# Kernel tuning notes

Measured on AMD Instinct MI355X. Metric: run time of the kernel, lower is better.

Reference implementation:

```python
import jax, jax.numpy as jnp
import numpy as np

ALPHA = 0.2          # LeakyReLU negative slope
NEG_BIG = -9e15      # mask value from original code


def setup_inputs() -> dict:
    key = jax.random.key(0)
    k1, k2, k3, k4 = jax.random.split(key, 4)
    B, N, F_in, F_out = 16, 1024, 256, 256
    x = jax.random.normal(k1, (B, N, F_in), dtype=jnp.float32)
    adj = jax.random.randint(k2, (B, N, N), 0, 2, dtype=jnp.int32)
    # xavier-uniform-like scales
    W = jax.random.normal(k3, (F_in, F_out), dtype=jnp.float32) * np.sqrt(2.0 / (F_in + F_out))
    a = jax.random.normal(k4, (2 * F_out, 1), dtype=jnp.float32) * np.sqrt(2.0 / (2 * F_out + 1))
    return {"x": x, "adj": adj, "W": W, "a": a}


def reference(x, adj, W, a):
    # x: [B,N,Fin], adj: [B,N,N] (int mask), W: [Fin,Fout], a: [2*Fout,1]
    F_out = a.shape[0] // 2
    h = jnp.einsum("bni,io->bno", x, W)            # [B,N,Fout]
    # Decompose a into left/right halves: e_ij = lrelu(a_l.h_i + a_r.h_j)
    a_l = a[:F_out, 0]                               # [Fout]
    a_r = a[F_out:, 0]                               # [Fout]
    el = h @ a_l                                     # [B,N] score contribution of target i
    er = h @ a_r                                     # [B,N] score contribution of source j
    e = jax.nn.leaky_relu(el[:, :, None] + er[:, None, :], ALPHA)  # [B,N,N]
    e = jnp.where(adj > 0, e, NEG_BIG)
    attn = jax.nn.softmax(e, axis=-1)                # masked softmax over neighbors j
    # weighted sum of neighbor features; concat with n_heads=1 is identity
    return jnp.einsum("bij,bjo->bio", attn, h)       # [B,N,Fout]
```

## Files before the change

### kernel.cpp

```cpp
#include <hip/hip_runtime.h>
#include <stdint.h>

#define ALPHA 0.2f
#define NEG_BIG -9000000000000000.0f
#define L2E 1.4426950408889634f

typedef __attribute__((ext_vector_type(8))) short bf16x8;
typedef __attribute__((ext_vector_type(8))) unsigned short u16x8;
typedef __attribute__((ext_vector_type(4))) float f32x4;

__device__ __forceinline__ unsigned short f2bf(float f) {
    unsigned int u = __float_as_uint(f);
    u += 0x7fffu + ((u >> 16) & 1u);
    return (unsigned short)(u >> 16);
}

__device__ __forceinline__ void gload_lds16(const void* g, void* l) {
    __builtin_amdgcn_global_load_lds(
        (const __attribute__((address_space(1))) unsigned int*)g,
        (__attribute__((address_space(3))) unsigned int*)l, 16, 0, 0);
}

__device__ __forceinline__ void bar_lds() {
    asm volatile("s_waitcnt lgkmcnt(0)" ::: "memory");
    __builtin_amdgcn_s_barrier();
}

__global__ void wt_wa_kernel(const float* __restrict__ W,
                             const float* __restrict__ a,
                             unsigned short* __restrict__ Wtbf,
                             float* __restrict__ wa) {
    const int t = threadIdx.x;
    if (blockIdx.x < 256) {
        const int o = blockIdx.x;
        Wtbf[o * 256 + t] = f2bf(W[t * 256 + o]);
    } else {
        float sl = 0.f, sr = 0.f;
        const float* wr = W + t * 256;
        for (int o = 0; o < 256; ++o) {
            const float wv = wr[o];
            sl += wv * a[o];
            sr += wv * a[256 + o];
        }
        wa[t] = sl;
        wa[256 + t] = sr;
    }
}

__global__ __launch_bounds__(256) void eler2x_kernel(
    const float* __restrict__ x, const float* __restrict__ wa,
    float* __restrict__ el, float* __restrict__ er,
    unsigned short* __restrict__ xbf)
{
    const int w = threadIdx.x >> 6, l = threadIdx.x & 63;
    const int r = blockIdx.x * 4 + w;
    const float4 xv = *(const float4*)(x + (size_t)r * 256 + l * 4);
    const float4 al = *(const float4*)(wa + l * 4);
    const float4 ar = *(const float4*)(wa + 256 + l * 4);

    ushort4 xb;
    xb.x = f2bf(xv.x); xb.y = f2bf(xv.y); xb.z = f2bf(xv.z); xb.w = f2bf(xv.w);
    *(ushort4*)(xbf + (size_t)r * 256 + l * 4) = xb;

    float sl = xv.x * al.x + xv.y * al.y + xv.z * al.z + xv.w * al.w;
    float sr = xv.x * ar.x + xv.y * ar.y + xv.z * ar.z + xv.w * ar.w;
#pragma unroll
    for (int off = 32; off >= 1; off >>= 1) {
        sl += __shfl_xor(sl, off);
        sr += __shfl_xor(sr, off);
    }
    if (l == 0) { el[r] = sl * L2E; er[r] = sr * L2E; }
}

__global__ __launch_bounds__(256) void gemm_h(
    const unsigned short* __restrict__ A,
    const unsigned short* __restrict__ Bt,
    unsigned short* __restrict__ C)
{
    __shared__ __align__(16) unsigned short As[64 * 64];
    __shared__ __align__(16) unsigned short Bs[128 * 64];

    const int tid = threadIdx.x;
    const int w = tid >> 6, l = tid & 63;
    const int q = l >> 4, ml = l & 15;
    const int wm = (w >> 1) * 32;
    const int wn = (w & 1) * 64;
    const int m0 = blockIdx.y * 64;
    const int n0 = blockIdx.x * 128;

    f32x4 acc[2][4];
    for (int i = 0; i < 2; ++i)
        for (int j = 0; j < 4; ++j) {
            f32x4 z = {0.f, 0.f, 0.f, 0.f};
            acc[i][j] = z;
        }

    for (int k0 = 0; k0 < 256; k0 += 64) {
        for (int c = 0; c < 2; ++c) {
            const int cb = c * 256 + (w << 6);
            const int p = cb + l;
            const int r = p >> 3;
            const int cc = (p & 7) ^ (r & 7);
            gload_lds16(A + (size_t)(m0 + r) * 256 + k0 + cc * 8, As + cb * 8);
        }
        for (int c = 0; c < 4; ++c) {
            const int cb = c * 256 + (w << 6);
            const int p = cb + l;
            const int r = p >> 3;
            const int cc = (p & 7) ^ (r & 7);
            gload_lds16(Bt + (size_t)(n0 + r) * 256 + k0 + cc * 8, Bs + cb * 8);
        }
        __syncthreads();

        bf16x8 aF[2][2], bF[2][4];
#pragma unroll
        for (int ks = 0; ks < 2; ++ks) {
#pragma unroll
            for (int mt = 0; mt < 2; ++mt) {
                const int mm = wm + mt * 16 + ml;
                aF[ks][mt] = *(const bf16x8*)(As + (mm * 8 + ((ks * 4 + q) ^ (mm & 7))) * 8);
            }
#pragma unroll
            for (int nt = 0; nt < 4; ++nt) {
                const int nn = wn + nt * 16 + ml;
                bF[ks][nt] = *(const bf16x8*)(Bs + (nn * 8 + ((ks * 4 + q) ^ (nn & 7))) * 8);
            }
        }
#pragma unroll
        for (int ks = 0; ks < 2; ++ks)
            for (int mt = 0; mt < 2; ++mt)
                for (int nt = 0; nt < 4; ++nt)
                    acc[mt][nt] = __builtin_amdgcn_mfma_f32_16x16x32_bf16(
                        aF[ks][mt], bF[ks][nt], acc[mt][nt], 0, 0, 0);
        __syncthreads();
    }

    for (int mt = 0; mt < 2; ++mt)
        for (int nt = 0; nt < 4; ++nt) {
            const int gn = n0 + wn + nt * 16 + ml;
            for (int r = 0; r < 4; ++r) {
                const int gm = m0 + wm + mt * 16 + q * 4 + r;
                C[(size_t)gm * 16384 + gn] = f2bf(acc[mt][nt][r]);
            }
        }
}

__global__ __launch_bounds__(256) void mask_kernel(
    const int* __restrict__ adj,
    const float* __restrict__ el,
    const float* __restrict__ er,
    float* __restrict__ c,
    unsigned short* __restrict__ pk16)
{
    __shared__ unsigned char nibs[4][256];

    const int w = threadIdx.x >> 6, l = threadIdx.x & 63;
    const int row = blockIdx.x * 4 + w;
    const int b = row >> 10;
    const int* arow = adj + (size_t)row * 1024;
    const float* erb = er + (b << 10);
    const float eli = el[row];

    float ev[16];
    float m = -3.0e38f;
#pragma unroll
    for (int it = 0; it < 4; ++it) {
        const int j = it * 256 + l * 4;
        const int4 av = *(const int4*)(arow + j);
        const float4 erv = *(const float4*)(erb + j);
        float e0 = eli + erv.x; e0 = e0 > 0.f ? e0 : ALPHA * e0; e0 = av.x > 0 ? e0 : NEG_BIG;
        float e1 = eli + erv.y; e1 = e1 > 0.f ? e1 : ALPHA * e1; e1 = av.y > 0 ? e1 : NEG_BIG;
        float e2 = eli + erv.z; e2 = e2 > 0.f ? e2 : ALPHA * e2; e2 = av.z > 0 ? e2 : NEG_BIG;
        float e3 = eli + erv.w; e3 = e3 > 0.f ? e3 : ALPHA * e3; e3 = av.w > 0 ? e3 : NEG_BIG;
        ev[it * 4 + 0] = e0; ev[it * 4 + 1] = e1;
        ev[it * 4 + 2] = e2; ev[it * 4 + 3] = e3;
        m = fmaxf(m, fmaxf(fmaxf(e0, e1), fmaxf(e2, e3)));
        nibs[w][it * 64 + l] =
            (unsigned char)((av.x > 0) | ((av.y > 0) << 1) |
                            ((av.z > 0) << 2) | ((av.w > 0) << 3));
    }
#pragma unroll
    for (int off = 32; off >= 1; off >>= 1) m = fmaxf(m, __shfl_xor(m, off));
    float s = 0.f;
#pragma unroll
    for (int u = 0; u < 16; ++u) s += exp2f(ev[u] - m);
#pragma unroll
    for (int off = 32; off >= 1; off >>= 1) s += __shfl_xor(s, off);
    if (l == 0) c[row] = m + log2f(s);

    const unsigned nr = *(const unsigned int*)(&nibs[w][l * 4]);
    const unsigned short mask16 =
        (unsigned short)((nr & 0xFu) | ((nr >> 4) & 0xF0u) |
                         ((nr >> 8) & 0xF00u) | ((nr >> 12) & 0xF000u));
    pk16[(size_t)row * 64 + l] = mask16;
}

__global__ __launch_bounds__(512, 2) void pv_kernel(
    const unsigned short* __restrict__ pk16,
    const float* __restrict__ el2,
    const float* __restrict__ er2,
    const float* __restrict__ c2,
    const unsigned short* __restrict__ hT,
    float* __restrict__ out)
{
    __shared__ float er_s[1024];
    __shared__ __align__(16) unsigned short pk_s[64 * 72];
    __shared__ __align__(16) unsigned short Ps[2 * 64 * 72];

    const int tid = threadIdx.x;
    const int w = tid >> 6, l = tid & 63;
    const int q = l >> 4, ml = l & 15;
    const int wm = (w >> 2) * 32;
    const int wn = (w & 3) * 64;

    const int lin = blockIdx.x;
    const int b = ((lin & 7) << 1) | ((lin >> 3) & 1);
    const int i0 = (lin >> 4) * 64;

    *(float2*)(er_s + tid * 2) = *(const float2*)(er2 + (b << 10) + tid * 2);
    {
        const int pr = tid >> 3, pc = (tid & 7) * 8;
        *(u16x8*)(pk_s + pr * 72 + pc) =
            *(const u16x8*)(pk16 + ((size_t)((b << 10) + i0 + pr)) * 64 + pc);
    }

    const int ib = tid >> 3;
    const int js = (tid & 7) * 8;
    const int rg = (b << 10) + i0 + ib;
    const float el2i = el2[rg];
    const float c2i = c2[rg];

    f32x4 acc[2][4];
#pragma unroll
    for (int i = 0; i < 2; ++i)
#pragma unroll
        for (int j = 0; j < 4; ++j) {
            f32x4 z = {0.f, 0.f, 0.f, 0.f};
            acc[i][j] = z;
        }

    const unsigned short* hb = hT + (size_t)b * 1024;
    const unsigned short* bp[4];
#pragma unroll
    for (int nt = 0; nt < 4; ++nt)
        bp[nt] = hb + (size_t)(wn + nt * 16 + ml) * 16384 + q * 8;

    bf16x8 B0[2][4], B1[2][4];

#define LOADB(B, t) do {                                                      \
    _Pragma("unroll")                                                         \
    for (int nt_ = 0; nt_ < 4; ++nt_) {                                       \
        B[0][nt_] = *(const bf16x8*)(bp[nt_] + (t) * 64);                     \
        B[1][nt_] = *(const bf16x8*)(bp[nt_] + (t) * 64 + 32);                \
    } } while (0)

#define BUILD(BI, t) do {                                                     \
    const int j0_ = (t) * 64;                                                 \
    float ev8[8];                                                             \
    *(f32x4*)(ev8)     = *(const f32x4*)(er_s + j0_ + js);                    \
    *(f32x4*)(ev8 + 4) = *(const f32x4*)(er_s + j0_ + js + 4);                \
    const unsigned hw_ = pk_s[ib * 72 + ((j0_ + js) >> 4)];                   \
    const unsigned mv_ = (hw_ >> (js & 8)) & 0xFFu;                           \
    u16x8 pv_;                                                                \
    _Pragma("unroll")                                                         \
    for (int u_ = 0; u_ < 8; ++u_) {                                          \
        float e_ = el2i + ev8[u_];                                            \
        e_ = fmaxf(e_, ALPHA * e_);         \
        float p_ = exp2f(e_ - c2i);                                           \
        p_ = ((mv_ >> u_) & 1u) ? p_ : 0.f;                                   \
        pv_[u_] = f2bf(p_);                                                   \
    }                                                                         \
    *(u16x8*)(Ps + (BI) * (64 * 72) + ib * 72 + js) = pv_;                    \
    } while (0)

#define COMPUTE(BI, B) do {                                                   \
    bf16x8 aF[2][2];                                                          \
    _Pragma("unroll")                                                         \
    for (int ks_ = 0; ks_ < 2; ++ks_)                                         \
        _Pragma("unroll")                                                     \
        for (int mt_ = 0; mt_ < 2; ++mt_)                                     \
            aF[ks_][mt_] = *(const bf16x8*)(Ps + (BI) * (64 * 72) +           \
                (wm + mt_ * 16 + ml) * 72 + ks_ * 32 + q * 8);                \
    _Pragma("unroll")                                                         \
    for (int ks_ = 0; ks_ < 2; ++ks_)                                         \
        _Pragma("unroll")                                                     \
        for (int mt_ = 0; mt_ < 2; ++mt_)                                     \
            _Pragma("unroll")                                                 \
            for (int nt_ = 0; nt_ < 4; ++nt_)                                 \
                acc[mt_][nt_] = __builtin_amdgcn_mfma_f32_16x16x32_bf16(      \
                    aF[ks_][mt_], B[ks_][nt_], acc[mt_][nt_], 0, 0, 0);       \
    } while (0)

    __syncthreads();
    LOADB(B0, 0);

    for (int t = 0; t < 16; t += 2) {
        BUILD(0, t);
        LOADB(B1, t + 1);
        bar_lds();
        COMPUTE(0, B0);
        BUILD(1, t + 1);
        if (t + 2 < 16) LOADB(B0, t + 2);
        bar_lds();
        COMPUTE(1, B1);
    }

#undef LOADB
#undef BUILD
#undef COMPUTE

    float* ob = out + (size_t)b * 262144;
#pragma unroll
    for (int mt = 0; mt < 2; ++mt)
#pragma unroll
        for (int nt = 0; nt < 4; ++nt) {
            const int gn = wn + nt * 16 + ml;
#pragma unroll
            for (int r = 0; r < 4; ++r) {
                const int gm = i0 + wm + mt * 16 + q * 4 + r;
                ob[(size_t)gm * 256 + gn] = acc[mt][nt][r];
            }
        }
}

extern "C" void kernel_launch(void* const* d_in, const int* in_sizes, int n_in,
                              void* d_out, int out_size, void* d_ws, size_t ws_size,
                              hipStream_t stream) {
    const float* x   = (const float*)d_in[0];
    const int*   adj = (const int*)d_in[1];
    const float* W   = (const float*)d_in[2];
    const float* a   = (const float*)d_in[3];
    float* out = (float*)d_out;

    char* ws = (char*)d_ws;
    unsigned short* Wtbf  = (unsigned short*)(ws);
    float* wa             = (float*)(ws + 131072);
    unsigned short* xbf   = (unsigned short*)(ws + 133120);
    unsigned short* h_T   = (unsigned short*)(ws + 8521728);
    float* el             = (float*)(ws + 16910336);
    float* er             = (float*)(ws + 16975872);
    float* c              = (float*)(ws + 17041408);
    unsigned short* pk16  = (unsigned short*)(ws + 17106944);

    wt_wa_kernel<<<dim3(257), dim3(256), 0, stream>>>(W, a, Wtbf, wa);

    eler2x_kernel<<<dim3(4096), dim3(256), 0, stream>>>(x, wa, el, er, xbf);

    gemm_h<<<dim3(128, 4), dim3(256), 0, stream>>>(Wtbf, xbf, h_T);

    mask_kernel<<<dim3(4096), dim3(256), 0, stream>>>(adj, el, er, c, pk16);

    pv_kernel<<<dim3(256), dim3(512), 0, stream>>>(pk16, el, er, c, h_T, out);
}
```

Measured before the change: 164.3 us.

## Double-buffer GEMM and PV kernels with async global-to-LDS staging

The h GEMM now double-buffers its A/B tiles, issuing the next k-slice's global-to-LDS loads before computing the current one and waiting with explicit vmcnt counts. The PV kernel stops loading h fragments straight into registers. It now stages 32-column h tiles into swizzled, double-buffered LDS through direct global-to-LDS loads, builds P in 32-wide chunks, and runs 32 iterations instead of 16. The block-to-batch mapping and launch bounds also change. This aims to hide global latency and cut register pressure, at the cost of more barriers per column of work and more LDS per block.

New measurement: 157.9 us. 1.04x faster.

```diff
diff --git a/kernel.cpp b/kernel.cpp
--- a/kernel.cpp
+++ b/kernel.cpp
@@ -19,11 +19,6 @@
     __builtin_amdgcn_global_load_lds(
         (const __attribute__((address_space(1))) unsigned int*)g,
         (__attribute__((address_space(3))) unsigned int*)l, 16, 0, 0);
-}
-
-__device__ __forceinline__ void bar_lds() {
-    asm volatile("s_waitcnt lgkmcnt(0)" ::: "memory");
-    __builtin_amdgcn_s_barrier();
 }
 
 __global__ void wt_wa_kernel(const float* __restrict__ W,
@@ -77,8 +72,8 @@
     const unsigned short* __restrict__ Bt,
     unsigned short* __restrict__ C)
 {
-    __shared__ __align__(16) unsigned short As[64 * 64];
-    __shared__ __align__(16) unsigned short Bs[128 * 64];
+    __shared__ __align__(16) unsigned short As[2 * 64 * 64];
+    __shared__ __align__(16) unsigned short Bs[2 * 128 * 64];
 
     const int tid = threadIdx.x;
     const int w = tid >> 6, l = tid & 63;
@@ -89,41 +84,61 @@
     const int n0 = blockIdx.x * 128;
 
     f32x4 acc[2][4];
+#pragma unroll
     for (int i = 0; i < 2; ++i)
+#pragma unroll
         for (int j = 0; j < 4; ++j) {
             f32x4 z = {0.f, 0.f, 0.f, 0.f};
             acc[i][j] = z;
         }
 
-    for (int k0 = 0; k0 < 256; k0 += 64) {
-        for (int c = 0; c < 2; ++c) {
-            const int cb = c * 256 + (w << 6);
-            const int p = cb + l;
-            const int r = p >> 3;
-            const int cc = (p & 7) ^ (r & 7);
-            gload_lds16(A + (size_t)(m0 + r) * 256 + k0 + cc * 8, As + cb * 8);
-        }
-        for (int c = 0; c < 4; ++c) {
-            const int cb = c * 256 + (w << 6);
-            const int p = cb + l;
-            const int r = p >> 3;
-            const int cc = (p & 7) ^ (r & 7);
-            gload_lds16(Bt + (size_t)(n0 + r) * 256 + k0 + cc * 8, Bs + cb * 8);
-        }
-        __syncthreads();
-
+#define GSTAGE(BI, K0) do {                                                   \
+    _Pragma("unroll")                                                         \
+    for (int c_ = 0; c_ < 2; ++c_) {                                          \
+        const int cb_ = c_ * 256 + (w << 6);                                  \
+        const int p_ = cb_ + l;                                               \
+        const int r_ = p_ >> 3;                                               \
+        const int cc_ = (p_ & 7) ^ (r_ & 7);                                  \
+        gload_lds16(A + (size_t)(m0 + r_) * 256 + (K0) + cc_ * 8,             \
+                    As + (BI) * 4096 + cb_ * 8);                              \
+    }                                                                         \
+    _Pragma("unroll")                                                         \
+    for (int c_ = 0; c_ < 4; ++c_) {                                          \
+        const int cb_ = c_ * 256 + (w << 6);                                  \
+        const int p_ = cb_ + l;                                               \
+        const int r_ = p_ >> 3;                                               \
+        const int cc_ = (p_ & 7) ^ (r_ & 7);                                  \
+        gload_lds16(Bt + (size_t)(n0 + r_) * 256 + (K0) + cc_ * 8,            \
+                    Bs + (BI) * 8192 + cb_ * 8);                              \
+    } } while (0)
+
+    GSTAGE(0, 0);
+
+    for (int s = 0; s < 4; ++s) {
+        const int cur = s & 1;
+        if (s + 1 < 4) {
+            GSTAGE((s + 1) & 1, (s + 1) * 64);
+            asm volatile("s_waitcnt vmcnt(6) lgkmcnt(0)" ::: "memory");
+        } else {
+            asm volatile("s_waitcnt vmcnt(0) lgkmcnt(0)" ::: "memory");
+        }
+        __builtin_amdgcn_s_barrier();
+        __builtin_amdgcn_sched_barrier(0);
+
+        const unsigned short* Ab = As + cur * 4096;
+        const unsigned short* Bb = Bs + cur * 8192;
         bf16x8 aF[2][2], bF[2][4];
 #pragma unroll
         for (int ks = 0; ks < 2; ++ks) {
 #pragma unroll
             for (int mt = 0; mt < 2; ++mt) {
                 const int mm = wm + mt * 16 + ml;
-                aF[ks][mt] = *(const bf16x8*)(As + (mm * 8 + ((ks * 4 + q) ^ (mm & 7))) * 8);
+                aF[ks][mt] = *(const bf16x8*)(Ab + (mm * 8 + ((ks * 4 + q) ^ (mm & 7))) * 8);
             }
 #pragma unroll
             for (int nt = 0; nt < 4; ++nt) {
                 const int nn = wn + nt * 16 + ml;
-                bF[ks][nt] = *(const bf16x8*)(Bs + (nn * 8 + ((ks * 4 + q) ^ (nn & 7))) * 8);
+                bF[ks][nt] = *(const bf16x8*)(Bb + (nn * 8 + ((ks * 4 + q) ^ (nn & 7))) * 8);
             }
         }
 #pragma unroll
@@ -132,8 +147,11 @@
                 for (int nt = 0; nt < 4; ++nt)
                     acc[mt][nt] = __builtin_amdgcn_mfma_f32_16x16x32_bf16(
                         aF[ks][mt], bF[ks][nt], acc[mt][nt], 0, 0, 0);
-        __syncthreads();
-    }
+
+        asm volatile("s_waitcnt lgkmcnt(0)" ::: "memory");
+        __builtin_amdgcn_s_barrier();
+    }
+#undef GSTAGE
 
     for (int mt = 0; mt < 2; ++mt)
         for (int nt = 0; nt < 4; ++nt) {
@@ -195,7 +213,7 @@
     pk16[(size_t)row * 64 + l] = mask16;
 }
 
-__global__ __launch_bounds__(512, 2) void pv_kernel(
+__global__ __launch_bounds__(512) void pv_kernel(
     const unsigned short* __restrict__ pk16,
     const float* __restrict__ el2,
     const float* __restrict__ er2,
@@ -204,8 +222,9 @@
     float* __restrict__ out)
 {
     __shared__ float er_s[1024];
-    __shared__ __align__(16) unsigned short pk_s[64 * 72];
-    __shared__ __align__(16) unsigned short Ps[2 * 64 * 72];
+    __shared__ __align__(16) unsigned short pk_s[64 * 64];
+    __shared__ __align__(16) unsigned short Hs[2 * 256 * 32];
+    __shared__ __align__(16) unsigned short Ps[2 * 64 * 40];
 
     const int tid = threadIdx.x;
     const int w = tid >> 6, l = tid & 63;
@@ -213,19 +232,17 @@
     const int wm = (w >> 2) * 32;
     const int wn = (w & 3) * 64;
 
-    const int lin = blockIdx.x;
-    const int b = ((lin & 7) << 1) | ((lin >> 3) & 1);
-    const int i0 = (lin >> 4) * 64;
+    const int bid = blockIdx.x;
+    const int slot = bid >> 3;
+    const int b = ((bid & 7) << 1) | (slot >> 4);
+    const int i0 = (slot & 15) * 64;
 
     *(float2*)(er_s + tid * 2) = *(const float2*)(er2 + (b << 10) + tid * 2);
-    {
-        const int pr = tid >> 3, pc = (tid & 7) * 8;
-        *(u16x8*)(pk_s + pr * 72 + pc) =
-            *(const u16x8*)(pk16 + ((size_t)((b << 10) + i0 + pr)) * 64 + pc);
-    }
+    *(u16x8*)(pk_s + (tid >> 3) * 64 + (tid & 7) * 8) =
+        *(const u16x8*)(pk16 + (size_t)((b << 10) + i0 + (tid >> 3)) * 64 + (tid & 7) * 8);
 
     const int ib = tid >> 3;
-    const int js = (tid & 7) * 8;
+    const int js = (tid & 7) * 4;
     const int rg = (b << 10) + i0 + ib;
     const float el2i = el2[rg];
     const float c2i = c2[rg];
@@ -240,72 +257,76 @@
         }
 
     const unsigned short* hb = hT + (size_t)b * 1024;
-    const unsigned short* bp[4];
-#pragma unroll
-    for (int nt = 0; nt < 4; ++nt)
-        bp[nt] = hb + (size_t)(wn + nt * 16 + ml) * 16384 + q * 8;
-
-    bf16x8 B0[2][4], B1[2][4];
-
-#define LOADB(B, t) do {                                                      \
+
+#define STAGE(BI, T) do {                                                     \
+    const int jb_ = (T) * 32;                                                 \
+    _Pragma("unroll")                                                         \
+    for (int c_ = 0; c_ < 2; ++c_) {                                          \
+        const int cb_ = c_ * 512 + (w << 6);                                  \
+        const int p_ = cb_ + l;                                               \
+        const int r_ = p_ >> 2;                                               \
+        const int cc_ = (p_ & 3) ^ ((r_ >> 1) & 3);                           \
+        gload_lds16(hb + (size_t)r_ * 16384 + jb_ + cc_ * 8,                  \
+                    Hs + (BI) * 8192 + cb_ * 8);                              \
+    } } while (0)
+
+#define BUILD(BI, T) do {                                                     \
+    const int jb_ = (T) * 32;                                                 \
+    const float4 ev_ = *(const float4*)(er_s + jb_ + js);                     \
+    const unsigned hw_ = pk_s[ib * 64 + ((jb_ + js) >> 4)];                   \
+    const unsigned mv_ = (hw_ >> (js & 12)) & 0xFu;                           \
+    float e0_ = el2i + ev_.x; e0_ = fmaxf(e0_, ALPHA * e0_);                  \
+    float e1_ = el2i + ev_.y; e1_ = fmaxf(e1_, ALPHA * e1_);                  \
+    float e2_ = el2i + ev_.z; e2_ = fmaxf(e2_, ALPHA * e2_);                  \
+    float e3_ = el2i + ev_.w; e3_ = fmaxf(e3_, ALPHA * e3_);                  \
+    ushort4 pv_;                                                              \
+    pv_.x = (mv_ & 1u) ? f2bf(exp2f(e0_ - c2i)) : (unsigned short)0;          \
+    pv_.y = (mv_ & 2u) ? f2bf(exp2f(e1_ - c2i)) : (unsigned short)0;          \
+    pv_.z = (mv_ & 4u) ? f2bf(exp2f(e2_ - c2i)) : (unsigned short)0;          \
+    pv_.w = (mv_ & 8u) ? f2bf(exp2f(e3_ - c2i)) : (unsigned short)0;          \
+    *(ushort4*)(Ps + (BI) * 2560 + ib * 40 + js) = pv_;                       \
+    } while (0)
+
+#define COMPUTE(BI) do {                                                      \
+    bf16x8 aF_[2], bF_[4];                                                    \
+    _Pragma("unroll")                                                         \
+    for (int mt_ = 0; mt_ < 2; ++mt_)                                         \
+        aF_[mt_] = *(const bf16x8*)(Ps + (BI) * 2560 +                        \
+                                    (wm + mt_ * 16 + ml) * 40 + q * 8);       \
     _Pragma("unroll")                                                         \
     for (int nt_ = 0; nt_ < 4; ++nt_) {                                       \
-        B[0][nt_] = *(const bf16x8*)(bp[nt_] + (t) * 64);                     \
-        B[1][nt_] = *(const bf16x8*)(bp[nt_] + (t) * 64 + 32);                \
-    } } while (0)
-
-#define BUILD(BI, t) do {                                                     \
-    const int j0_ = (t) * 64;                                                 \
-    float ev8[8];                                                             \
-    *(f32x4*)(ev8)     = *(const f32x4*)(er_s + j0_ + js);                    \
-    *(f32x4*)(ev8 + 4) = *(const f32x4*)(er_s + j0_ + js + 4);                \
-    const unsigned hw_ = pk_s[ib * 72 + ((j0_ + js) >> 4)];                   \
-    const unsigned mv_ = (hw_ >> (js & 8)) & 0xFFu;                           \
-    u16x8 pv_;                                                                \
-    _Pragma("unroll")                                                         \
-    for (int u_ = 0; u_ < 8; ++u_) {                                          \
-        float e_ = el2i + ev8[u_];                                            \
-        e_ = fmaxf(e_, ALPHA * e_);         \
-        float p_ = exp2f(e_ - c2i);                                           \
-        p_ = ((mv_ >> u_) & 1u) ? p_ : 0.f;                                   \
-        pv_[u_] = f2bf(p_);                                                   \
+        const int oc_ = wn + nt_ * 16 + ml;                                   \
+        const int sl_ = q ^ ((oc_ >> 1) & 3);                                 \
+        bF_[nt_] = *(const bf16x8*)(Hs + (BI) * 8192 + oc_ * 32 + sl_ * 8);   \
     }                                                                         \
-    *(u16x8*)(Ps + (BI) * (64 * 72) + ib * 72 + js) = pv_;                    \
+    _Pragma("unroll")                                                         \
+    for (int mt_ = 0; mt_ < 2; ++mt_)                                         \
+        _Pragma("unroll")                                                     \
+        for (int nt_ = 0; nt_ < 4; ++nt_)                                     \
+            acc[mt_][nt_] = __builtin_amdgcn_mfma_f32_16x16x32_bf16(          \
+                aF_[mt_], bF_[nt_], acc[mt_][nt_], 0, 0, 0);                  \
     } while (0)
 
-#define COMPUTE(BI, B) do {                                                   \
-    bf16x8 aF[2][2];                                                          \
-    _Pragma("unroll")                                                         \
-    for (int ks_ = 0; ks_ < 2; ++ks_)                                         \
-        _Pragma("unroll")                                                     \
-        for (int mt_ = 0; mt_ < 2; ++mt_)                                     \
-            aF[ks_][mt_] = *(const bf16x8*)(Ps + (BI) * (64 * 72) +           \
-                (wm + mt_ * 16 + ml) * 72 + ks_ * 32 + q * 8);                \
-    _Pragma("unroll")                                                         \
-    for (int ks_ = 0; ks_ < 2; ++ks_)                                         \
-        _Pragma("unroll")                                                     \
-        for (int mt_ = 0; mt_ < 2; ++mt_)                                     \
-            _Pragma("unroll")                                                 \
-            for (int nt_ = 0; nt_ < 4; ++nt_)                                 \
-                acc[mt_][nt_] = __builtin_amdgcn_mfma_f32_16x16x32_bf16(      \
-                    aF[ks_][mt_], B[ks_][nt_], acc[mt_][nt_], 0, 0, 0);       \
-    } while (0)
-
-    __syncthreads();
-    LOADB(B0, 0);
-
-    for (int t = 0; t < 16; t += 2) {
-        BUILD(0, t);
-        LOADB(B1, t + 1);
-        bar_lds();
-        COMPUTE(0, B0);
-        BUILD(1, t + 1);
-        if (t + 2 < 16) LOADB(B0, t + 2);
-        bar_lds();
-        COMPUTE(1, B1);
-    }
-
-#undef LOADB
+    STAGE(0, 0);
+    asm volatile("s_waitcnt lgkmcnt(0)" ::: "memory");
+    __builtin_amdgcn_s_barrier();
+
+    for (int t = 0; t < 32; ++t) {
+        const int cur = t & 1;
+        if (t + 1 < 32) STAGE((t + 1) & 1, t + 1);
+        BUILD(cur, t);
+        if (t + 1 < 32)
+            asm volatile("s_waitcnt vmcnt(2) lgkmcnt(0)" ::: "memory");
+        else
+            asm volatile("s_waitcnt vmcnt(0) lgkmcnt(0)" ::: "memory");
+        __builtin_amdgcn_s_barrier();
+        __builtin_amdgcn_sched_barrier(0);
+        COMPUTE(cur);
+        asm volatile("s_waitcnt lgkmcnt(0)" ::: "memory");
+        __builtin_amdgcn_s_barrier();
+    }
+
+#undef STAGE
 #undef BUILD
 #undef COMPUTE
 
```
